# Performance work log

Hardware: AMD Instinct MI355X
Metric: run time of the kernel (lower is better)

## Reference

```python
import jax, jax.numpy as jnp
import numpy as np

THRESHOLD = 0.5
NEG_POS_RATIO = 3
ALPHA = 1.0
B, P, C, O = 128, 8732, 21, 32


def xy_to_cxcy(xy):
    return jnp.concatenate([(xy[..., 2:] + xy[..., :2]) / 2, xy[..., 2:] - xy[..., :2]], axis=-1)


def cxcy_to_xy(cxcy):
    return jnp.concatenate([cxcy[..., :2] - cxcy[..., 2:] / 2, cxcy[..., :2] + cxcy[..., 2:] / 2], axis=-1)


def cxcy_to_gcxgcy(cxcy, priors_cxcy):
    g_cxcy = (cxcy[..., :2] - priors_cxcy[..., :2]) / (priors_cxcy[..., 2:] / 10.0)
    g_wh = jnp.log(cxcy[..., 2:] / priors_cxcy[..., 2:]) * 5.0
    return jnp.concatenate([g_cxcy, g_wh], axis=-1)


def find_jaccard_overlap(set1, set2):
    # set1: [O,4] xy, set2: [P,4] xy -> [O,P]
    lo = jnp.maximum(set1[:, None, :2], set2[None, :, :2])
    hi = jnp.minimum(set1[:, None, 2:], set2[None, :, 2:])
    inter = jnp.prod(jnp.clip(hi - lo, 0.0), axis=-1)
    a1 = jnp.prod(set1[:, 2:] - set1[:, :2], axis=-1)
    a2 = jnp.prod(set2[:, 2:] - set2[:, :2], axis=-1)
    union = a1[:, None] + a2[None, :] - inter
    return inter / union


def setup_inputs() -> dict:
    key = jax.random.key(0)
    k0, k1, k2, k3, k4, k5, k6 = jax.random.split(key, 7)
    predicted_locs = jax.random.normal(k0, (B, P, 4), jnp.float32)
    predicted_scores = jax.random.normal(k1, (B, P, C), jnp.float32)
    centers = jax.random.uniform(k2, (B, O, 2), jnp.float32, 0.2, 0.8)
    sizes = jax.random.uniform(k3, (B, O, 2), jnp.float32, 0.05, 0.3)
    boxes = jnp.concatenate([centers - sizes / 2, centers + sizes / 2], axis=-1)
    labels = jax.random.randint(k4, (B, O), 0, C)
    p_c = jax.random.uniform(k5, (P, 2), jnp.float32, 0.05, 0.95)
    p_wh = jax.random.uniform(k6, (P, 2), jnp.float32, 0.05, 0.5)
    priors_cxcy = jnp.concatenate([p_c, p_wh], axis=-1)
    return {"predicted_locs": predicted_locs, "predicted_scores": predicted_scores,
            "boxes": boxes, "labels": labels, "priors_cxcy": priors_cxcy}


def reference(predicted_locs, predicted_scores, boxes, labels, priors_cxcy):
    priors_xy = cxcy_to_xy(priors_cxcy)

    def match_one(boxes_i, labels_i):
        overlap = find_jaccard_overlap(boxes_i, priors_xy)           # [O,P]
        overlap_for_each_prior = jnp.max(overlap, axis=0)            # [P]
        object_for_each_prior = jnp.argmax(overlap, axis=0)          # [P]
        prior_for_each_object = jnp.argmax(overlap, axis=1)          # [O]
        object_for_each_prior = object_for_each_prior.at[prior_for_each_object].set(jnp.arange(O))
        overlap_for_each_prior = overlap_for_each_prior.at[prior_for_each_object].set(1.0)
        label_for_each_prior = labels_i[object_for_each_prior]
        label_for_each_prior = jnp.where(overlap_for_each_prior < THRESHOLD, 0, label_for_each_prior)
        true_locs_i = cxcy_to_gcxgcy(xy_to_cxcy(boxes_i[object_for_each_prior]), priors_cxcy)
        return label_for_each_prior, true_locs_i

    true_classes, true_locs = jax.vmap(match_one)(boxes, labels)     # [B,P], [B,P,4]

    positive = true_classes != 0                                     # [B,P]
    n_positives = jnp.sum(positive, axis=1)                          # [B]
    n_pos_total = jnp.sum(n_positives)

    # L1Loss (mean over selected positive elements, 4 per prior)
    abs_diff = jnp.abs(predicted_locs - true_locs)                   # [B,P,4]
    loc_loss = jnp.sum(abs_diff * positive[..., None]) / (n_pos_total.astype(jnp.float32) * 4.0)

    # per-element cross-entropy
    log_p = jax.nn.log_softmax(predicted_scores, axis=-1)            # [B,P,C]
    conf_loss_all = -jnp.take_along_axis(log_p, true_classes[..., None], axis=-1)[..., 0]  # [B,P]

    conf_loss_pos_sum = jnp.sum(jnp.where(positive, conf_loss_all, 0.0))
    conf_loss_neg = jnp.where(positive, 0.0, conf_loss_all)
    conf_loss_neg_sorted = -jnp.sort(-conf_loss_neg, axis=1)         # descending
    n_hard = NEG_POS_RATIO * n_positives                             # [B]
    hard_mask = jnp.arange(P)[None, :] < n_hard[:, None]             # [B,P]
    conf_loss_hard_neg_sum = jnp.sum(jnp.where(hard_mask, conf_loss_neg_sorted, 0.0))

    conf_loss = (conf_loss_hard_neg_sum + conf_loss_pos_sum) / n_pos_total.astype(jnp.float32)
    return conf_loss + ALPHA * loc_loss
```

## Files before the change

kernel.cpp:

```cpp
#include <hip/hip_runtime.h>
#include <hip/hip_bf16.h>

#define NB 128
#define NP 8732
#define NO 32
#define NC 21


__global__ __launch_bounds__(256) void k_init(int* ws) {
    int i = blockIdx.x * 256 + threadIdx.x;
    const int n = 36352 / 4;
    if (i < n) ws[i] = 0;
}

__global__ __launch_bounds__(256) void k_match(const float* __restrict__ boxes,
                                               const float* __restrict__ priors,
                                               int* __restrict__ code,
                                               unsigned long long* __restrict__ packed) {
    int b = blockIdx.y;
    int tid = threadIdx.x;
    int base = blockIdx.x * 1024 + tid;
    int lane = tid & 63;

    __shared__ float4 sbox[NO];
    if (tid < NO)
        sbox[tid] = ((const float4*)(boxes + (size_t)b * NO * 4))[tid];
    __syncthreads();

    float px1[4], py1[4], px2[4], py2[4], pa[4];
    float bestv[4];
    int   besto[4];
#pragma unroll
    for (int j = 0; j < 4; ++j) {
        int p = base + 256 * j;
        int pp = p < NP ? p : NP - 1;
        float4 pr = ((const float4*)priors)[pp];
        px1[j] = pr.x - pr.z * 0.5f; py1[j] = pr.y - pr.w * 0.5f;
        px2[j] = pr.x + pr.z * 0.5f; py2[j] = pr.y + pr.w * 0.5f;
        pa[j]  = (px2[j] - px1[j]) * (py2[j] - py1[j]);
        bestv[j] = -1.0f; besto[j] = 0;
    }

    int wavep0 = blockIdx.x * 1024 + (tid & ~63);

#pragma unroll 2
    for (int o = 0; o < NO; ++o) {
        float4 bx = sbox[o];
        float a1 = (bx.z - bx.x) * (bx.w - bx.y);
        float iou[4];
#pragma unroll
        for (int j = 0; j < 4; ++j) {
            float lx = fmaxf(bx.x, px1[j]), ly = fmaxf(bx.y, py1[j]);
            float hx = fminf(bx.z, px2[j]), hy = fminf(bx.w, py2[j]);
            float iw = fmaxf(hx - lx, 0.0f), ih = fmaxf(hy - ly, 0.0f);
            float inter = iw * ih;
            iou[j] = inter / (a1 + pa[j] - inter);
            if (iou[j] > bestv[j]) { bestv[j] = iou[j]; besto[j] = o; }
        }
        float m = fmaxf(fmaxf(iou[0], iou[1]), fmaxf(iou[2], iou[3]));
        for (int s = 32; s > 0; s >>= 1)
            m = fmaxf(m, __shfl_xor(m, s, 64));
        unsigned long long b0 = __ballot(iou[0] == m);
        unsigned long long b1 = __ballot(iou[1] == m);
        unsigned long long b2 = __ballot(iou[2] == m);
        unsigned long long b3 = __ballot(iou[3] == m);
        if (lane == 0) {
            unsigned long long bb; int jj;
            if (b0)      { bb = b0; jj = 0; }
            else if (b1) { bb = b1; jj = 1; }
            else if (b2) { bb = b2; jj = 2; }
            else         { bb = b3; jj = 3; }
            unsigned p = (unsigned)(wavep0 + 256 * jj) + (unsigned)(__ffsll(bb) - 1);
            unsigned long long key =
                ((unsigned long long)__float_as_uint(m) << 32) |
                (unsigned long long)(0xFFFFFFFFu - p);
            atomicMax(&packed[b * NO + o], key);
        }
    }
#pragma unroll
    for (int j = 0; j < 4; ++j) {
        int p = base + 256 * j;
        if (p < NP)
            code[(size_t)b * NP + p] = besto[j] | (bestv[j] >= 0.5f ? 256 : 0);
    }
}

__global__ void k_force(int* __restrict__ code,
                        const unsigned long long* __restrict__ packed) {
    int b = threadIdx.x;
    if (b >= NB) return;
    for (int o = 0; o < NO; ++o) {
        unsigned long long pk = packed[b * NO + o];
        unsigned p = 0xFFFFFFFFu - (unsigned)(pk & 0xFFFFFFFFull);
        if (p < NP) code[(size_t)b * NP + p] = o | 256;
    }
}

__global__ __launch_bounds__(256) void k_loss(const float* __restrict__ plocs,
                                              const float* __restrict__ scores,
                                              const float* __restrict__ boxes,
                                              const int* __restrict__ labels,
                                              const float* __restrict__ priors,
                                              const int* __restrict__ code,
                                              float* __restrict__ confneg,
                                              int* __restrict__ npos,
                                              double* __restrict__ accb) {
    __shared__ float srow[256 * NC];
    int b = blockIdx.y;
    int p0 = blockIdx.x * 256;
    int cnt = NP - p0; if (cnt > 256) cnt = 256;
    int nf4 = cnt * NC / 4;
    const float4* src4 = (const float4*)(scores + ((size_t)b * NP + p0) * NC);
    for (int i = threadIdx.x; i < nf4; i += 256)
        ((float4*)srow)[i] = src4[i];
    __syncthreads();

    int p = p0 + threadIdx.x;
    float posconf = 0.0f, locpart = 0.0f;
    int isp = 0;

    if (p < NP) {
        int cd = code[(size_t)b * NP + p];
        int obj = cd & 255;
        int lbl = (cd & 256) ? labels[b * NO + obj] : 0;

        const float* s = srow + threadIdx.x * NC;
        float m = s[0];
#pragma unroll
        for (int c = 1; c < NC; ++c) m = fmaxf(m, s[c]);
        float sum = 0.0f;
#pragma unroll
        for (int c = 0; c < NC; ++c) sum += __expf(s[c] - m);
        float conf = m + __logf(sum) - s[lbl];

        if (lbl != 0) {
            isp = 1;
            posconf = conf;
            float4 bx = ((const float4*)boxes)[b * NO + obj];
            float4 pr = ((const float4*)priors)[p];
            float cx = (bx.x + bx.z) * 0.5f, cy = (bx.y + bx.w) * 0.5f;
            float w = bx.z - bx.x, h = bx.w - bx.y;
            float gx = (cx - pr.x) / (pr.z * 0.1f);
            float gy = (cy - pr.y) / (pr.w * 0.1f);
            float gw = __logf(w / pr.z) * 5.0f;
            float gh = __logf(h / pr.w) * 5.0f;
            float4 pl = ((const float4*)plocs)[(size_t)b * NP + p];
            locpart = fabsf(pl.x - gx) + fabsf(pl.y - gy) +
                      fabsf(pl.z - gw) + fabsf(pl.w - gh);
        }
        confneg[(size_t)b * NP + p] = isp ? 0.0f : conf;
    }

    for (int s = 32; s > 0; s >>= 1) {
        posconf += __shfl_xor(posconf, s, 64);
        locpart += __shfl_xor(locpart, s, 64);
        isp     += __shfl_xor(isp, s, 64);
    }
    __shared__ float w0[4], w1[4];
    __shared__ int wc[4];
    int wid = threadIdx.x >> 6, lane = threadIdx.x & 63;
    if (lane == 0) { w0[wid] = posconf; w1[wid] = locpart; wc[wid] = isp; }
    __syncthreads();
    if (threadIdx.x == 0) {
        float t0 = w0[0] + w0[1] + w0[2] + w0[3];
        float t1 = w1[0] + w1[1] + w1[2] + w1[3];
        int   tc = wc[0] + wc[1] + wc[2] + wc[3];
        atomicAdd(&npos[b], tc);
        atomicAdd(&accb[b * 3 + 0], (double)t0);
        atomicAdd(&accb[b * 3 + 1], (double)t1);
    }
}

__global__ __launch_bounds__(1024) void k_topk(const float* __restrict__ confneg,
                                               const int* __restrict__ npos,
                                               double* __restrict__ accb) {
    __shared__ int   si[16];
    __shared__ double sd[16];
    __shared__ int   sbcast;
    int tid = threadIdx.x, b = blockIdx.x;
    int lane = tid & 63, wid = tid >> 6;

    const float* src = confneg + (size_t)b * NP;
    float val[9];
#pragma unroll
    for (int j = 0; j < 9; ++j) {
        int i = tid + j * 1024;
        val[j] = (i < NP) ? src[i] : 0.0f;
    }
    int k = npos[b] * 3;
    if (k > NP) k = NP;
    if (k <= 0) return;

    unsigned T = 0;
    for (int bit = 30; bit >= 0; --bit) {
        unsigned cand = T | (1u << bit);
        int cnt = 0;
#pragma unroll
        for (int j = 0; j < 9; ++j)
            cnt += (__float_as_uint(val[j]) >= cand) ? 1 : 0;
        for (int s = 32; s > 0; s >>= 1) cnt += __shfl_xor(cnt, s, 64);
        if (lane == 0) si[wid] = cnt;
        __syncthreads();
        if (tid == 0) {
            int t = 0;
            for (int w = 0; w < 16; ++w) t += si[w];
            sbcast = t;
        }
        __syncthreads();
        if (sbcast >= k) T = cand;
    }

    int cgt = 0;
    double sgt = 0.0;
#pragma unroll
    for (int j = 0; j < 9; ++j) {
        unsigned u = __float_as_uint(val[j]);
        if (u > T) { cgt++; sgt += (double)val[j]; }
    }
    for (int s = 32; s > 0; s >>= 1) {
        cgt += __shfl_xor(cgt, s, 64);
        sgt += __shfl_xor(sgt, s, 64);
    }
    if (lane == 0) { si[wid] = cgt; sd[wid] = sgt; }
    __syncthreads();
    if (tid == 0) {
        int cg = 0; double sg = 0.0;
        for (int w = 0; w < 16; ++w) { cg += si[w]; sg += sd[w]; }
        accb[b * 3 + 2] = sg + (double)(k - cg) * (double)__uint_as_float(T);
    }
}

__global__ __launch_bounds__(128) void k_final(const int* __restrict__ npos,
                                               const double* __restrict__ accb,
                                               float* __restrict__ out) {
    int b = threadIdx.x;
    double pc = accb[b * 3 + 0];
    double lc = accb[b * 3 + 1];
    double hn = accb[b * 3 + 2];
    double np_ = (double)npos[b];
    for (int s = 32; s > 0; s >>= 1) {
        pc  += __shfl_xor(pc, s, 64);
        lc  += __shfl_xor(lc, s, 64);
        hn  += __shfl_xor(hn, s, 64);
        np_ += __shfl_xor(np_, s, 64);
    }
    __shared__ double sD[4][2];
    int wid = threadIdx.x >> 6, lane = threadIdx.x & 63;
    if (lane == 0) { sD[0][wid] = pc; sD[1][wid] = lc; sD[2][wid] = hn; sD[3][wid] = np_; }
    __syncthreads();
    if (threadIdx.x == 0) {
        double P = sD[0][0] + sD[0][1];
        double L = sD[1][0] + sD[1][1];
        double H = sD[2][0] + sD[2][1];
        double nt = sD[3][0] + sD[3][1];
        out[0] = (float)((H + P) / nt + L / (nt * 4.0));
    }
}

extern "C" void kernel_launch(void* const* d_in, const int* in_sizes, int n_in,
                              void* d_out, int out_size, void* d_ws, size_t ws_size,
                              hipStream_t stream) {
    const float* plocs  = (const float*)d_in[0];
    const float* scores = (const float*)d_in[1];
    const float* boxes  = (const float*)d_in[2];
    const int*   labels = (const int*)d_in[3];
    const float* priors = (const float*)d_in[4];
    float* out = (float*)d_out;

    char* ws = (char*)d_ws;
    unsigned long long* packed = (unsigned long long*)ws;
    int*    npos    = (int*)(ws + 32768);
    double* accb    = (double*)(ws + 33280);
    int*    code    = (int*)(ws + 36352);
    float*  confneg = (float*)(ws + 36352 + (size_t)NB * NP * 4);

    hipLaunchKernelGGL(k_init, dim3((36352 / 4 + 255) / 256), dim3(256), 0, stream, (int*)ws);
    hipLaunchKernelGGL(k_match, dim3((NP + 1023) / 1024, NB), dim3(256), 0, stream,
                       boxes, priors, code, packed);
    hipLaunchKernelGGL(k_force, dim3(1), dim3(128), 0, stream, code, packed);
    hipLaunchKernelGGL(k_loss, dim3((NP + 255) / 256, NB), dim3(256), 0, stream,
                       plocs, scores, boxes, labels, priors, code, confneg, npos, accb);
    hipLaunchKernelGGL(k_topk, dim3(NB), dim3(1024), 0, stream, confneg, npos, accb);
    hipLaunchKernelGGL(k_final, dim3(1), dim3(128), 0, stream, npos, accb, out);
}
```

Baseline: 247.7 us.

## Fold forced-match and final reduction into neighbor kernels; decouple match reductions

Removes the single-block k_force kernel by having k_loss read the per-object best-prior indices from the packed array into shared memory and override matches there. Removes k_final by having the last k_topk block, found through an atomic done counter, perform the final reduction. k_match now handles 2 priors per thread instead of 4, doubling the grid. It also computes all 32 IoUs first and then runs the wave max-reductions in a separate loop, which adds a 32-entry register array. This cuts two serial launches, including a slow 1-block kernel, at the cost of more register pressure and a 32-compare loop per prior in k_loss.

Measured after the change: 296.5 us. 19.7% more time.

```diff
diff --git a/kernel.cpp b/kernel.cpp
--- a/kernel.cpp
+++ b/kernel.cpp
@@ -9,7 +9,7 @@
 
 __global__ __launch_bounds__(256) void k_init(int* ws) {
     int i = blockIdx.x * 256 + threadIdx.x;
-    const int n = 36352 / 4;
+    const int n = 36608 / 4;
     if (i < n) ws[i] = 0;
 }
 
@@ -19,80 +19,79 @@
                                                unsigned long long* __restrict__ packed) {
     int b = blockIdx.y;
     int tid = threadIdx.x;
-    int base = blockIdx.x * 1024 + tid;
     int lane = tid & 63;
+    int bb = blockIdx.x * 512;
 
     __shared__ float4 sbox[NO];
     if (tid < NO)
         sbox[tid] = ((const float4*)(boxes + (size_t)b * NO * 4))[tid];
     __syncthreads();
 
-    float px1[4], py1[4], px2[4], py2[4], pa[4];
-    float bestv[4];
-    int   besto[4];
-#pragma unroll
-    for (int j = 0; j < 4; ++j) {
-        int p = base + 256 * j;
+    float px1[2], py1[2], px2[2], py2[2], pa[2];
+#pragma unroll
+    for (int j = 0; j < 2; ++j) {
+        int p = bb + 256 * j + tid;
         int pp = p < NP ? p : NP - 1;
         float4 pr = ((const float4*)priors)[pp];
         px1[j] = pr.x - pr.z * 0.5f; py1[j] = pr.y - pr.w * 0.5f;
         px2[j] = pr.x + pr.z * 0.5f; py2[j] = pr.y + pr.w * 0.5f;
         pa[j]  = (px2[j] - px1[j]) * (py2[j] - py1[j]);
-        bestv[j] = -1.0f; besto[j] = 0;
-    }
-
-    int wavep0 = blockIdx.x * 1024 + (tid & ~63);
-
-#pragma unroll 2
+    }
+
+    float bestv0 = -1.0f, bestv1 = -1.0f;
+    int   besto0 = 0,     besto1 = 0;
+    float locmax[NO];
+    unsigned f0 = 0u, f1 = 0u;
+
+#pragma unroll
     for (int o = 0; o < NO; ++o) {
         float4 bx = sbox[o];
         float a1 = (bx.z - bx.x) * (bx.w - bx.y);
-        float iou[4];
-#pragma unroll
-        for (int j = 0; j < 4; ++j) {
-            float lx = fmaxf(bx.x, px1[j]), ly = fmaxf(bx.y, py1[j]);
-            float hx = fminf(bx.z, px2[j]), hy = fminf(bx.w, py2[j]);
-            float iw = fmaxf(hx - lx, 0.0f), ih = fmaxf(hy - ly, 0.0f);
-            float inter = iw * ih;
-            iou[j] = inter / (a1 + pa[j] - inter);
-            if (iou[j] > bestv[j]) { bestv[j] = iou[j]; besto[j] = o; }
-        }
-        float m = fmaxf(fmaxf(iou[0], iou[1]), fmaxf(iou[2], iou[3]));
+
+        float lx0 = fmaxf(bx.x, px1[0]), ly0 = fmaxf(bx.y, py1[0]);
+        float hx0 = fminf(bx.z, px2[0]), hy0 = fminf(bx.w, py2[0]);
+        float in0 = fmaxf(hx0 - lx0, 0.0f) * fmaxf(hy0 - ly0, 0.0f);
+        float i0  = in0 / (a1 + pa[0] - in0);
+
+        float lx1 = fmaxf(bx.x, px1[1]), ly1 = fmaxf(bx.y, py1[1]);
+        float hx1 = fminf(bx.z, px2[1]), hy1 = fminf(bx.w, py2[1]);
+        float in1 = fmaxf(hx1 - lx1, 0.0f) * fmaxf(hy1 - ly1, 0.0f);
+        float i1  = in1 / (a1 + pa[1] - in1);
+
+        if (i0 > bestv0) { bestv0 = i0; besto0 = o; }
+        if (i1 > bestv1) { bestv1 = i1; besto1 = o; }
+
+        float lm = fmaxf(i0, i1);
+        locmax[o] = lm;
+        f0 |= (i0 == lm ? 1u : 0u) << o;
+        f1 |= (i1 == lm ? 1u : 0u) << o;
+    }
+
+    int wl0 = bb + (tid & ~63);
+
+#pragma unroll
+    for (int o = 0; o < NO; ++o) {
+        float m = locmax[o];
         for (int s = 32; s > 0; s >>= 1)
             m = fmaxf(m, __shfl_xor(m, s, 64));
-        unsigned long long b0 = __ballot(iou[0] == m);
-        unsigned long long b1 = __ballot(iou[1] == m);
-        unsigned long long b2 = __ballot(iou[2] == m);
-        unsigned long long b3 = __ballot(iou[3] == m);
+        unsigned long long b0 = __ballot(((f0 >> o) & 1u) && (locmax[o] == m));
+        unsigned long long b1 = __ballot(((f1 >> o) & 1u) && (locmax[o] == m));
         if (lane == 0) {
-            unsigned long long bb; int jj;
-            if (b0)      { bb = b0; jj = 0; }
-            else if (b1) { bb = b1; jj = 1; }
-            else if (b2) { bb = b2; jj = 2; }
-            else         { bb = b3; jj = 3; }
-            unsigned p = (unsigned)(wavep0 + 256 * jj) + (unsigned)(__ffsll(bb) - 1);
+            unsigned p;
+            if (b0) p = (unsigned)(wl0 + (__ffsll((unsigned long long)b0) - 1));
+            else    p = (unsigned)(wl0 + 256 + (__ffsll((unsigned long long)b1) - 1));
             unsigned long long key =
                 ((unsigned long long)__float_as_uint(m) << 32) |
                 (unsigned long long)(0xFFFFFFFFu - p);
             atomicMax(&packed[b * NO + o], key);
         }
     }
-#pragma unroll
-    for (int j = 0; j < 4; ++j) {
-        int p = base + 256 * j;
-        if (p < NP)
-            code[(size_t)b * NP + p] = besto[j] | (bestv[j] >= 0.5f ? 256 : 0);
-    }
-}
-
-__global__ void k_force(int* __restrict__ code,
-                        const unsigned long long* __restrict__ packed) {
-    int b = threadIdx.x;
-    if (b >= NB) return;
-    for (int o = 0; o < NO; ++o) {
-        unsigned long long pk = packed[b * NO + o];
-        unsigned p = 0xFFFFFFFFu - (unsigned)(pk & 0xFFFFFFFFull);
-        if (p < NP) code[(size_t)b * NP + p] = o | 256;
+
+    {
+        int p0 = bb + tid;
+        int p1 = bb + 256 + tid;
+        if (p0 < NP) code[(size_t)b * NP + p0] = besto0 | (bestv0 >= 0.5f ? 256 : 0);
+        if (p1 < NP) code[(size_t)b * NP + p1] = besto1 | (bestv1 >= 0.5f ? 256 : 0);
     }
 }
 
@@ -102,10 +101,12 @@
                                               const int* __restrict__ labels,
                                               const float* __restrict__ priors,
                                               const int* __restrict__ code,
+                                              const unsigned long long* __restrict__ packed,
                                               float* __restrict__ confneg,
                                               int* __restrict__ npos,
                                               double* __restrict__ accb) {
     __shared__ float srow[256 * NC];
+    __shared__ unsigned spfl[NO];
     int b = blockIdx.y;
     int p0 = blockIdx.x * 256;
     int cnt = NP - p0; if (cnt > 256) cnt = 256;
@@ -113,6 +114,10 @@
     const float4* src4 = (const float4*)(scores + ((size_t)b * NP + p0) * NC);
     for (int i = threadIdx.x; i < nf4; i += 256)
         ((float4*)srow)[i] = src4[i];
+    if (threadIdx.x < NO) {
+        unsigned long long pk = packed[b * NO + threadIdx.x];
+        spfl[threadIdx.x] = 0xFFFFFFFFu - (unsigned)(pk & 0xFFFFFFFFull);
+    }
     __syncthreads();
 
     int p = p0 + threadIdx.x;
@@ -122,7 +127,11 @@
     if (p < NP) {
         int cd = code[(size_t)b * NP + p];
         int obj = cd & 255;
-        int lbl = (cd & 256) ? labels[b * NO + obj] : 0;
+        int mat = cd >> 8;
+#pragma unroll
+        for (int o = 0; o < NO; ++o)
+            if (spfl[o] == (unsigned)p) { obj = o; mat = 1; }
+        int lbl = mat ? labels[b * NO + obj] : 0;
 
         const float* s = srow + threadIdx.x * NC;
         float m = s[0];
@@ -173,7 +182,9 @@
 
 __global__ __launch_bounds__(1024) void k_topk(const float* __restrict__ confneg,
                                                const int* __restrict__ npos,
-                                               double* __restrict__ accb) {
+                                               double* __restrict__ accb,
+                                               int* __restrict__ donecnt,
+                                               float* __restrict__ out) {
     __shared__ int   si[16];
     __shared__ double sd[16];
     __shared__ int   sbcast;
@@ -189,70 +200,80 @@
     }
     int k = npos[b] * 3;
     if (k > NP) k = NP;
-    if (k <= 0) return;
-
-    unsigned T = 0;
-    for (int bit = 30; bit >= 0; --bit) {
-        unsigned cand = T | (1u << bit);
-        int cnt = 0;
-#pragma unroll
-        for (int j = 0; j < 9; ++j)
-            cnt += (__float_as_uint(val[j]) >= cand) ? 1 : 0;
-        for (int s = 32; s > 0; s >>= 1) cnt += __shfl_xor(cnt, s, 64);
-        if (lane == 0) si[wid] = cnt;
+
+    if (k > 0) {
+        unsigned T = 0;
+        for (int bit = 30; bit >= 0; --bit) {
+            unsigned cand = T | (1u << bit);
+            int cnt = 0;
+#pragma unroll
+            for (int j = 0; j < 9; ++j)
+                cnt += (__float_as_uint(val[j]) >= cand) ? 1 : 0;
+            for (int s = 32; s > 0; s >>= 1) cnt += __shfl_xor(cnt, s, 64);
+            if (lane == 0) si[wid] = cnt;
+            __syncthreads();
+            if (tid == 0) {
+                int t = 0;
+                for (int w = 0; w < 16; ++w) t += si[w];
+                sbcast = t;
+            }
+            __syncthreads();
+            if (sbcast >= k) T = cand;
+        }
+
+        int cgt = 0;
+        double sgt = 0.0;
+#pragma unroll
+        for (int j = 0; j < 9; ++j) {
+            unsigned u = __float_as_uint(val[j]);
+            if (u > T) { cgt++; sgt += (double)val[j]; }
+        }
+        for (int s = 32; s > 0; s >>= 1) {
+            cgt += __shfl_xor(cgt, s, 64);
+            sgt += __shfl_xor(sgt, s, 64);
+        }
+        if (lane == 0) { si[wid] = cgt; sd[wid] = sgt; }
         __syncthreads();
         if (tid == 0) {
-            int t = 0;
-            for (int w = 0; w < 16; ++w) t += si[w];
-            sbcast = t;
-        }
-        __syncthreads();
-        if (sbcast >= k) T = cand;
-    }
-
-    int cgt = 0;
-    double sgt = 0.0;
-#pragma unroll
-    for (int j = 0; j < 9; ++j) {
-        unsigned u = __float_as_uint(val[j]);
-        if (u > T) { cgt++; sgt += (double)val[j]; }
-    }
-    for (int s = 32; s > 0; s >>= 1) {
-        cgt += __shfl_xor(cgt, s, 64);
-        sgt += __shfl_xor(sgt, s, 64);
-    }
-    if (lane == 0) { si[wid] = cgt; sd[wid] = sgt; }
-    __syncthreads();
+            int cg = 0; double sg = 0.0;
+            for (int w = 0; w < 16; ++w) { cg += si[w]; sg += sd[w]; }
+            accb[b * 3 + 2] = sg + (double)(k - cg) * (double)__uint_as_float(T);
+        }
+    }
+
+    __shared__ int samlast;
     if (tid == 0) {
-        int cg = 0; double sg = 0.0;
-        for (int w = 0; w < 16; ++w) { cg += si[w]; sg += sd[w]; }
-        accb[b * 3 + 2] = sg + (double)(k - cg) * (double)__uint_as_float(T);
-    }
-}
-
-__global__ __launch_bounds__(128) void k_final(const int* __restrict__ npos,
-                                               const double* __restrict__ accb,
-                                               float* __restrict__ out) {
-    int b = threadIdx.x;
-    double pc = accb[b * 3 + 0];
-    double lc = accb[b * 3 + 1];
-    double hn = accb[b * 3 + 2];
-    double np_ = (double)npos[b];
-    for (int s = 32; s > 0; s >>= 1) {
-        pc  += __shfl_xor(pc, s, 64);
-        lc  += __shfl_xor(lc, s, 64);
-        hn  += __shfl_xor(hn, s, 64);
-        np_ += __shfl_xor(np_, s, 64);
-    }
-    __shared__ double sD[4][2];
-    int wid = threadIdx.x >> 6, lane = threadIdx.x & 63;
-    if (lane == 0) { sD[0][wid] = pc; sD[1][wid] = lc; sD[2][wid] = hn; sD[3][wid] = np_; }
-    __syncthreads();
-    if (threadIdx.x == 0) {
-        double P = sD[0][0] + sD[0][1];
-        double L = sD[1][0] + sD[1][1];
-        double H = sD[2][0] + sD[2][1];
-        double nt = sD[3][0] + sD[3][1];
+        __threadfence();
+        int prev = atomicAdd(donecnt, 1);
+        samlast = (prev == NB - 1) ? 1 : 0;
+    }
+    __syncthreads();
+    if (!samlast) return;
+    __threadfence();
+
+    double pc = 0.0, lc = 0.0, hn = 0.0, np_ = 0.0;
+    if (tid < NB) {
+        pc  = accb[tid * 3 + 0];
+        lc  = accb[tid * 3 + 1];
+        hn  = atomicAdd(&accb[tid * 3 + 2], 0.0);
+        np_ = (double)npos[tid];
+    }
+    if (tid < 128) {
+        for (int s = 32; s > 0; s >>= 1) {
+            pc  += __shfl_xor(pc, s, 64);
+            lc  += __shfl_xor(lc, s, 64);
+            hn  += __shfl_xor(hn, s, 64);
+            np_ += __shfl_xor(np_, s, 64);
+        }
+        if (lane == 0) { sd[wid * 4 + 0] = pc; sd[wid * 4 + 1] = lc;
+                         sd[wid * 4 + 2] = hn; sd[wid * 4 + 3] = np_; }
+    }
+    __syncthreads();
+    if (tid == 0) {
+        double P = sd[0] + sd[4];
+        double L = sd[1] + sd[5];
+        double H = sd[2] + sd[6];
+        double nt = sd[3] + sd[7];
         out[0] = (float)((H + P) / nt + L / (nt * 4.0));
     }
 }
@@ -271,15 +292,14 @@
     unsigned long long* packed = (unsigned long long*)ws;
     int*    npos    = (int*)(ws + 32768);
     double* accb    = (double*)(ws + 33280);
-    int*    code    = (int*)(ws + 36352);
-    float*  confneg = (float*)(ws + 36352 + (size_t)NB * NP * 4);
-
-    hipLaunchKernelGGL(k_init, dim3((36352 / 4 + 255) / 256), dim3(256), 0, stream, (int*)ws);
-    hipLaunchKernelGGL(k_match, dim3((NP + 1023) / 1024, NB), dim3(256), 0, stream,
+    int*    donecnt = (int*)(ws + 36352);
+    int*    code    = (int*)(ws + 36608);
+    float*  confneg = (float*)(ws + 36608 + (size_t)NB * NP * 4);
+
+    hipLaunchKernelGGL(k_init, dim3((36608 / 4 + 255) / 256), dim3(256), 0, stream, (int*)ws);
+    hipLaunchKernelGGL(k_match, dim3((NP + 511) / 512, NB), dim3(256), 0, stream,
                        boxes, priors, code, packed);
-    hipLaunchKernelGGL(k_force, dim3(1), dim3(128), 0, stream, code, packed);
     hipLaunchKernelGGL(k_loss, dim3((NP + 255) / 256, NB), dim3(256), 0, stream,
-                       plocs, scores, boxes, labels, priors, code, confneg, npos, accb);
-    hipLaunchKernelGGL(k_topk, dim3(NB), dim3(1024), 0, stream, confneg, npos, accb);
-    hipLaunchKernelGGL(k_final, dim3(1), dim3(128), 0, stream, npos, accb, out);
-}
+                       plocs, scores, boxes, labels, priors, code, packed, confneg, npos, accb);
+    hipLaunchKernelGGL(k_topk, dim3(NB), dim3(1024), 0, stream, confneg, npos, accb, donecnt, out);
+}
```
